# Kernel tuning notes

Hardware: AMD Instinct MI355X
Metric: run time of the kernel (lower is better)

The kernel has to match this reference:

```python
import jax, jax.numpy as jnp
import numpy as np


def setup_inputs() -> dict:
    key = jax.random.key(0)
    k1, k2, k3, k4 = jax.random.split(key, 4)
    B, K, M, X, Y = 64, 4, 3, 256, 256
    predictions = jax.random.uniform(k1, (B, K, X, Y), dtype=jnp.float32)
    inputs = jax.random.normal(k2, (B, M, X, Y), dtype=jnp.float32)
    heart = jax.random.randint(k3, (B, 1, X, Y), 0, 2, dtype=jnp.int32)
    mu_data = jax.random.normal(k4, (K, M), dtype=jnp.float32)
    return {"predictions": predictions, "inputs": inputs, "heart": heart, "mu_data": mu_data}


def reference(predictions, inputs, heart, mu_data):
    eps = 1e-10
    # Boolean-mask gather is equivalent to multiplying by the 0/1 mask, since
    # everything downstream is a sum over the masked positions.
    mask = (heart[:, 0] == 1).astype(predictions.dtype)          # [B, X, Y]
    pm = predictions * mask[:, None]                             # [B, K, X, Y]
    num = jnp.einsum('bkxy,bmxy->bkm', pm, inputs)               # weighted sums
    den = jnp.sum(pm, axis=(2, 3)) + eps                         # [B, K]
    mu_mean = jnp.mean(num / den[..., None], axis=0)             # [K, M]
    return jnp.sum((mu_data - mu_mean) ** 2)
```

## Files before the change

### kernel.cpp

```cpp
#include <hip/hip_runtime.h>

#define B_    64
#define K_    4
#define M_    3
#define NPIX  65536
#define CHUNKS 64
#define TPB   256
#define NV    16

__global__ __launch_bounds__(TPB) void partial_kernel(
    const float* __restrict__ pred,
    const float* __restrict__ inp,
    const int*   __restrict__ heart,
    float* __restrict__ num_ws,
    float* __restrict__ den_ws)
{
    const int b     = blockIdx.x >> 6;
    const int chunk = blockIdx.x & 63;
    const int pix   = chunk * (NPIX / CHUNKS) + (int)threadIdx.x * 4;

    const int4 h = *reinterpret_cast<const int4*>(heart + (size_t)b * NPIX + pix);
    float4 mask;
    mask.x = (h.x == 1) ? 1.0f : 0.0f;
    mask.y = (h.y == 1) ? 1.0f : 0.0f;
    mask.z = (h.z == 1) ? 1.0f : 0.0f;
    mask.w = (h.w == 1) ? 1.0f : 0.0f;

    float4 in[M_];
#pragma unroll
    for (int m = 0; m < M_; ++m)
        in[m] = *reinterpret_cast<const float4*>(inp + ((size_t)b * M_ + m) * NPIX + pix);

    float val[NV];
#pragma unroll
    for (int k = 0; k < K_; ++k) {
        float4 p = *reinterpret_cast<const float4*>(pred + ((size_t)b * K_ + k) * NPIX + pix);
        float4 pm;
        pm.x = p.x * mask.x; pm.y = p.y * mask.y;
        pm.z = p.z * mask.z; pm.w = p.w * mask.w;
        val[k] = (pm.x + pm.y) + (pm.z + pm.w);
#pragma unroll
        for (int m = 0; m < M_; ++m)
            val[4 + k * M_ + m] = pm.x * in[m].x + pm.y * in[m].y
                                + pm.z * in[m].z + pm.w * in[m].w;
    }

#pragma unroll
    for (int off = 32; off > 0; off >>= 1) {
#pragma unroll
        for (int i = 0; i < NV; ++i)
            val[i] += __shfl_down(val[i], off, 64);
    }

    __shared__ float smem[TPB / 64][NV];
    const int lane = threadIdx.x & 63;
    const int wave = threadIdx.x >> 6;
    if (lane == 0) {
#pragma unroll
        for (int i = 0; i < NV; ++i) smem[wave][i] = val[i];
    }
    __syncthreads();

    if (threadIdx.x < NV) {
        float s = smem[0][threadIdx.x] + smem[1][threadIdx.x]
                + smem[2][threadIdx.x] + smem[3][threadIdx.x];
        if (threadIdx.x < K_)
            atomicAdd(&den_ws[b * K_ + threadIdx.x], s);
        else
            atomicAdd(&num_ws[b * (K_ * M_) + (threadIdx.x - K_)], s);
    }
}

__global__ __launch_bounds__(64) void finalize_kernel(
    const float* __restrict__ num_ws,
    const float* __restrict__ den_ws,
    const float* __restrict__ mu_data,
    float* __restrict__ out)
{
    const int b = threadIdx.x;
    float r[K_ * M_];
#pragma unroll
    for (int k = 0; k < K_; ++k) {
        const float den = den_ws[b * K_ + k] + 1e-10f;
        const float inv = 1.0f / den;
#pragma unroll
        for (int m = 0; m < M_; ++m)
            r[k * M_ + m] = num_ws[b * (K_ * M_) + k * M_ + m] * inv;
    }
#pragma unroll
    for (int off = 32; off > 0; off >>= 1) {
#pragma unroll
        for (int i = 0; i < K_ * M_; ++i)
            r[i] += __shfl_down(r[i], off, 64);
    }
    if (b == 0) {
        float s = 0.0f;
#pragma unroll
        for (int i = 0; i < K_ * M_; ++i) {
            const float d = mu_data[i] - r[i] * (1.0f / (float)B_);
            s += d * d;
        }
        out[0] = s;
    }
}

extern "C" void kernel_launch(void* const* d_in, const int* in_sizes, int n_in,
                              void* d_out, int out_size, void* d_ws, size_t ws_size,
                              hipStream_t stream) {
    const float* pred    = (const float*)d_in[0];
    const float* inp     = (const float*)d_in[1];
    const int*   heart   = (const int*)d_in[2];
    const float* mu_data = (const float*)d_in[3];
    float* out = (float*)d_out;

    float* num_ws = (float*)d_ws;
    float* den_ws = num_ws + B_ * K_ * M_;

    hipMemsetAsync(d_ws, 0, (size_t)(B_ * K_ * M_ + B_ * K_) * sizeof(float), stream);

    partial_kernel<<<B_ * CHUNKS, TPB, 0, stream>>>(pred, inp, heart, num_ws, den_ws);
    finalize_kernel<<<1, 64, 0, stream>>>(num_ws, den_ws, mu_data, out);
}
```

Before: 150.1 us.

## Process four pixel tiles per thread and replace atomics with per-chunk partials

Each block now covers four times as many pixels, with each thread accumulating four float4 groups in registers. This cuts the grid from 4096 to 1024 blocks and reduces the shuffle/shared-memory reductions per pixel. Atomic adds and the workspace memset are replaced by plain stores of per-chunk partials, which the finalize kernel sums serially. The trade-off is fewer blocks in flight for hiding memory latency, plus a serial 16-chunk loop in finalize.

```diff
diff --git a/kernel.cpp b/kernel.cpp
--- a/kernel.cpp
+++ b/kernel.cpp
@@ -1,48 +1,56 @@
 #include <hip/hip_runtime.h>
 
-#define B_    64
-#define K_    4
-#define M_    3
-#define NPIX  65536
-#define CHUNKS 64
-#define TPB   256
-#define NV    16
+#define B_      64
+#define K_      4
+#define M_      3
+#define NPIX    65536
+#define CHUNKS  16
+#define TPB     256
+#define ITERS   4
+#define NV      16
 
-__global__ __launch_bounds__(TPB) void partial_kernel(
+__global__ __launch_bounds__(TPB, 4) void partial_kernel(
     const float* __restrict__ pred,
     const float* __restrict__ inp,
     const int*   __restrict__ heart,
-    float* __restrict__ num_ws,
-    float* __restrict__ den_ws)
+    float* __restrict__ partial_ws)
 {
-    const int b     = blockIdx.x >> 6;
-    const int chunk = blockIdx.x & 63;
-    const int pix   = chunk * (NPIX / CHUNKS) + (int)threadIdx.x * 4;
-
-    const int4 h = *reinterpret_cast<const int4*>(heart + (size_t)b * NPIX + pix);
-    float4 mask;
-    mask.x = (h.x == 1) ? 1.0f : 0.0f;
-    mask.y = (h.y == 1) ? 1.0f : 0.0f;
-    mask.z = (h.z == 1) ? 1.0f : 0.0f;
-    mask.w = (h.w == 1) ? 1.0f : 0.0f;
-
-    float4 in[M_];
-#pragma unroll
-    for (int m = 0; m < M_; ++m)
-        in[m] = *reinterpret_cast<const float4*>(inp + ((size_t)b * M_ + m) * NPIX + pix);
+    const int c = blockIdx.x;
+    const int b = blockIdx.y;
+    const int base = c * (NPIX / CHUNKS) + (int)threadIdx.x * 4;
 
     float val[NV];
 #pragma unroll
-    for (int k = 0; k < K_; ++k) {
-        float4 p = *reinterpret_cast<const float4*>(pred + ((size_t)b * K_ + k) * NPIX + pix);
-        float4 pm;
-        pm.x = p.x * mask.x; pm.y = p.y * mask.y;
-        pm.z = p.z * mask.z; pm.w = p.w * mask.w;
-        val[k] = (pm.x + pm.y) + (pm.z + pm.w);
+    for (int i = 0; i < NV; ++i) val[i] = 0.0f;
+
+#pragma unroll
+    for (int it = 0; it < ITERS; ++it) {
+        const int pix = base + it * (TPB * 4);
+
+        const int4 h = *reinterpret_cast<const int4*>(heart + (size_t)b * NPIX + pix);
+        float4 mask;
+        mask.x = (h.x == 1) ? 1.0f : 0.0f;
+        mask.y = (h.y == 1) ? 1.0f : 0.0f;
+        mask.z = (h.z == 1) ? 1.0f : 0.0f;
+        mask.w = (h.w == 1) ? 1.0f : 0.0f;
+
+        float4 in[M_];
 #pragma unroll
         for (int m = 0; m < M_; ++m)
-            val[4 + k * M_ + m] = pm.x * in[m].x + pm.y * in[m].y
-                                + pm.z * in[m].z + pm.w * in[m].w;
+            in[m] = *reinterpret_cast<const float4*>(inp + ((size_t)b * M_ + m) * NPIX + pix);
+
+#pragma unroll
+        for (int k = 0; k < K_; ++k) {
+            float4 p = *reinterpret_cast<const float4*>(pred + ((size_t)b * K_ + k) * NPIX + pix);
+            float4 pm;
+            pm.x = p.x * mask.x; pm.y = p.y * mask.y;
+            pm.z = p.z * mask.z; pm.w = p.w * mask.w;
+            val[k] += (pm.x + pm.y) + (pm.z + pm.w);
+#pragma unroll
+            for (int m = 0; m < M_; ++m)
+                val[4 + k * M_ + m] += pm.x * in[m].x + pm.y * in[m].y
+                                     + pm.z * in[m].z + pm.w * in[m].w;
+        }
     }
 
 #pragma unroll
@@ -62,30 +70,34 @@
     __syncthreads();
 
     if (threadIdx.x < NV) {
-        float s = smem[0][threadIdx.x] + smem[1][threadIdx.x]
-                + smem[2][threadIdx.x] + smem[3][threadIdx.x];
-        if (threadIdx.x < K_)
-            atomicAdd(&den_ws[b * K_ + threadIdx.x], s);
-        else
-            atomicAdd(&num_ws[b * (K_ * M_) + (threadIdx.x - K_)], s);
+        const float s = smem[0][threadIdx.x] + smem[1][threadIdx.x]
+                      + smem[2][threadIdx.x] + smem[3][threadIdx.x];
+        partial_ws[((size_t)b * CHUNKS + c) * NV + threadIdx.x] = s;
     }
 }
 
 __global__ __launch_bounds__(64) void finalize_kernel(
-    const float* __restrict__ num_ws,
-    const float* __restrict__ den_ws,
+    const float* __restrict__ partial_ws,
     const float* __restrict__ mu_data,
     float* __restrict__ out)
 {
     const int b = threadIdx.x;
+    float acc[NV];
+#pragma unroll
+    for (int i = 0; i < NV; ++i) acc[i] = 0.0f;
+    for (int c = 0; c < CHUNKS; ++c) {
+        const float* p = partial_ws + ((size_t)b * CHUNKS + c) * NV;
+#pragma unroll
+        for (int i = 0; i < NV; ++i) acc[i] += p[i];
+    }
+
     float r[K_ * M_];
 #pragma unroll
     for (int k = 0; k < K_; ++k) {
-        const float den = den_ws[b * K_ + k] + 1e-10f;
-        const float inv = 1.0f / den;
+        const float inv = 1.0f / (acc[k] + 1e-10f);
 #pragma unroll
         for (int m = 0; m < M_; ++m)
-            r[k * M_ + m] = num_ws[b * (K_ * M_) + k * M_ + m] * inv;
+            r[k * M_ + m] = acc[4 + k * M_ + m] * inv;
     }
 #pragma unroll
     for (int off = 32; off > 0; off >>= 1) {
@@ -113,11 +125,9 @@
     const float* mu_data = (const float*)d_in[3];
     float* out = (float*)d_out;
 
-    float* num_ws = (float*)d_ws;
-    float* den_ws = num_ws + B_ * K_ * M_;
+    float* partial_ws = (float*)d_ws;
 
-    hipMemsetAsync(d_ws, 0, (size_t)(B_ * K_ * M_ + B_ * K_) * sizeof(float), stream);
-
-    partial_kernel<<<B_ * CHUNKS, TPB, 0, stream>>>(pred, inp, heart, num_ws, den_ws);
-    finalize_kernel<<<1, 64, 0, stream>>>(num_ws, den_ws, mu_data, out);
+    dim3 grid(CHUNKS, B_);
+    partial_kernel<<<grid, TPB, 0, stream>>>(pred, inp, heart, partial_ws);
+    finalize_kernel<<<1, 64, 0, stream>>>(partial_ws, mu_data, out);
 }
```

Result: slower. 168.9 us (+12.5%).
